# Kernel tuning notes

Measured on AMD Instinct MI355X. Metric: run time of the kernel, lower is better.

The kernel has to match this reference:

```python
import jax, jax.numpy as jnp
import numpy as np

B, T, HW = 16, 64, 7
D = 768          # input_dim == base_dim
N = 12           # num_heads
C = D // N       # head_dim = 64
EPS = 1e-5


def layernorm(x, g, b):
    m = jnp.mean(x, axis=-1, keepdims=True)
    v = jnp.mean((x - m) ** 2, axis=-1, keepdims=True)
    return (x - m) * jax.lax.rsqrt(v + EPS) * g + b


def setup_inputs() -> dict:
    key = jax.random.key(0)
    ks = jax.random.split(key, 12)
    s = lambda k, shape: (jax.random.normal(k, shape, jnp.float32) * 0.02)
    return {
        "x": jax.random.normal(ks[0], (B, T, HW, HW, D), jnp.float32),
        "W_qkv": s(ks[1], (D, 3 * D)),                  # qkv_bias=False
        "Wpq": s(ks[2], (C, C, HW, HW)), "bpq": jnp.zeros((C,), jnp.float32),
        "Wpk": s(ks[3], (C, C, HW, HW)), "bpk": jnp.zeros((C,), jnp.float32),
        "Wpv": s(ks[4], (C, C, HW, HW)), "bpv": jnp.zeros((C,), jnp.float32),
        "g_q": jnp.ones((C,), jnp.float32), "be_q": jnp.zeros((C,), jnp.float32),
        "g_k": jnp.ones((C,), jnp.float32), "be_k": jnp.zeros((C,), jnp.float32),
        "g_v": jnp.ones((C,), jnp.float32), "be_v": jnp.zeros((C,), jnp.float32),
        "rel_pos_t": s(ks[5], (2 * T - 1, C)),          # (127, 64): matches dt, no interp
        "W_proj": s(ks[6], (D, D)), "b_proj": jnp.zeros((D,), jnp.float32),
    }


def reference(x, W_qkv, Wpq, bpq, Wpk, bpk, Wpv, bpv,
              g_q, be_q, g_k, be_k, g_v, be_v, rel_pos_t, W_proj, b_proj):
    b, t = x.shape[0], x.shape[1]
    # qkv projection -> (B,T,H,W,3,N,C)
    qkv = (x @ W_qkv).reshape(b, t, HW, HW, 3, N, C)
    q3, k3, v3 = qkv[..., 0, :, :], qkv[..., 1, :, :], qkv[..., 2, :, :]  # (B,T,H,W,N,C)
    # Conv3d kernel (1,7,7) on full 7x7 spatial == contraction over (h,w,c_in)
    q = jnp.einsum('bthwnc,dchw->bntd', q3, Wpq) + bpq   # (B,N,T,C)
    k = jnp.einsum('bthwnc,dchw->bntd', k3, Wpk) + bpk
    v = jnp.einsum('bthwnc,dchw->bntd', v3, Wpv) + bpv
    q = layernorm(q, g_q, be_q)
    k = layernorm(k, g_k, be_k)
    v = layernorm(v, g_v, be_v)
    scale = C ** -0.5
    attn = jnp.einsum('bntc,bnsc->bnts', q * scale, k)   # (B,N,T,T)
    # relative temporal position bias: gather table rows by distance, matmul with q
    dist = jnp.arange(t)[:, None] - jnp.arange(t)[None, :] + (t - 1)  # (T,T) in [0,2T-2]
    Rt = rel_pos_t[dist]                                  # (T,T,C)
    rel = jnp.einsum('bntc,tsc->bnts', q, Rt)
    attn = jax.nn.softmax(attn + rel, axis=-1)
    out = jnp.einsum('bnts,bnsc->bntc', attn, v) + q      # residual add of q
    out = out.transpose(0, 2, 1, 3).reshape(b, t, N * C)  # (B,T,D)
    return out @ W_proj + b_proj
```

## Files before the change

kernel.cpp:

```cpp
#include <hip/hip_runtime.h>


typedef __attribute__((ext_vector_type(8))) short bf16x8;
typedef __attribute__((ext_vector_type(4))) float f32x4;

#define AS1U(p) ((const __attribute__((address_space(1))) unsigned int*)(p))
#define AS3U(p) ((__attribute__((address_space(3))) unsigned int*)(p))

__device__ __forceinline__ unsigned short cvt_bf16(float x) {
  union { float f; unsigned int u; } v; v.f = x;
  unsigned int r = v.u + 0x7fffu + ((v.u >> 16) & 1u);
  return (unsigned short)(r >> 16);
}
__device__ __forceinline__ float bf2f(unsigned short h) {
  union { unsigned int u; float f; } v; v.u = ((unsigned int)h) << 16;
  return v.f;
}

__device__ __forceinline__ void wg_barrier() {
  asm volatile("" ::: "memory");
  __builtin_amdgcn_s_barrier();
  asm volatile("" ::: "memory");
}

__global__ __launch_bounds__(256) void cvt_x_k(const float* __restrict__ src,
                                               unsigned short* __restrict__ dst, int n8) {
  int i = blockIdx.x * 256 + threadIdx.x;
  if (i >= n8) return;
  const float4* s = (const float4*)src + (size_t)i * 2;
  float4 a = s[0], b = s[1];
  ushort4 r0 = { cvt_bf16(a.x), cvt_bf16(a.y), cvt_bf16(a.z), cvt_bf16(a.w) };
  ushort4 r1 = { cvt_bf16(b.x), cvt_bf16(b.y), cvt_bf16(b.z), cvt_bf16(b.w) };
  ushort4* d = (ushort4*)dst + (size_t)i * 2;
  d[0] = r0; d[1] = r1;
}

__global__ __launch_bounds__(256) void transpose_cvt_k(const float* __restrict__ src,
                                                       unsigned short* __restrict__ dst) {
  __shared__ float tl[32][33];
  int k0 = blockIdx.x * 32, n0 = blockIdx.y * 32;
  int tx = threadIdx.x & 31, ty = threadIdx.x >> 5;
#pragma unroll
  for (int r = 0; r < 32; r += 8)
    tl[ty + r][tx] = src[(size_t)(k0 + ty + r) * 2304 + n0 + tx];
  __syncthreads();
#pragma unroll
  for (int r = 0; r < 32; r += 8)
    dst[(size_t)(n0 + ty + r) * 768 + k0 + tx] = cvt_bf16(tl[tx][ty + r]);
}

__global__ __launch_bounds__(256) void wp_cvt_k(const float* __restrict__ src,
                                                unsigned short* __restrict__ dst) {
  int o = blockIdx.x * 256 + threadIdx.x;
  if (o >= 204800) return;
  int c = o & 63, d = (o >> 6) & 63, hw = o >> 12;
  dst[o] = (hw < 49) ? cvt_bf16(src[d * 3136 + c * 49 + hw]) : (unsigned short)0;
}

__global__ __launch_bounds__(256) void relp_cvt_k(const float* __restrict__ src,
                                                  unsigned short* __restrict__ dst) {
  int i = blockIdx.x * 256 + threadIdx.x;
  if (i >= 8192) return;
  dst[i] = (i < 8128) ? cvt_bf16(src[i]) : (unsigned short)0;
}

__global__ __launch_bounds__(512, 2) void gemm_qkv_8ph(
    const unsigned short* __restrict__ A, const unsigned short* __restrict__ Bt,
    unsigned short* __restrict__ Cb) {
  __shared__ unsigned short As[2][16384];
  __shared__ unsigned short Bs[2][16384];

  const int orig = blockIdx.x;
  const int xcd = orig & 7;
  const int lid = orig >> 3;
  const int wgid = (xcd < 4 ? xcd * 221 : 884 + (xcd - 4) * 220) + lid;
  const int mb = wgid / 9, nb = wgid % 9;
  const int m0 = mb * 256, n0 = nb * 256;
  const int K = 768;

  const int tid = threadIdx.x;
  const int wave = tid >> 6, lane = tid & 63;
  const int quad = lane >> 4, l16 = lane & 15;
  const int wr = wave >> 2, wc = wave & 3;
  const int x7 = l16 & 7;

  const int srow = tid >> 3;
  const int cs = (tid & 7) ^ (srow & 7);
  const unsigned short* Ag[4];
  const unsigned short* Bg[4];
#pragma unroll
  for (int l = 0; l < 4; ++l) {
    Ag[l] = A + (size_t)(m0 + l * 64 + srow) * K + cs * 8;
    Bg[l] = Bt + (size_t)(n0 + l * 64 + srow) * K + cs * 8;
  }
  const int ldst = wave * 512;

#define STAGE(buf, kt) do {                                                        \
    const int ko_ = (kt) * 64;                                                     \
    _Pragma("unroll")                                                              \
    for (int l_ = 0; l_ < 4; ++l_) {                                               \
      __builtin_amdgcn_global_load_lds(AS1U(Ag[l_] + ko_),                         \
          AS3U(&As[buf][l_ * 4096 + ldst]), 16, 0, 0);                             \
      __builtin_amdgcn_global_load_lds(AS1U(Bg[l_] + ko_),                         \
          AS3U(&Bs[buf][l_ * 4096 + ldst]), 16, 0, 0);                             \
    }                                                                              \
  } while (0)

#define LDA(buf, mi) do {                                                          \
    _Pragma("unroll")                                                              \
    for (int fi_ = 0; fi_ < 4; ++fi_) {                                            \
      const int row_ = wr * 128 + (mi) * 64 + fi_ * 16 + l16;                      \
      _Pragma("unroll")                                                            \
      for (int ks_ = 0; ks_ < 2; ++ks_)                                            \
        af[fi_][ks_] = *(const bf16x8*)&As[buf][row_ * 64 +                        \
            (((ks_ * 4 + quad) ^ x7) * 8)];                                        \
    }                                                                              \
  } while (0)

#define LDB(buf, nj) do {                                                          \
    _Pragma("unroll")                                                              \
    for (int fj_ = 0; fj_ < 2; ++fj_) {                                            \
      const int row_ = wc * 64 + (nj) * 32 + fj_ * 16 + l16;                       \
      _Pragma("unroll")                                                            \
      for (int ks_ = 0; ks_ < 2; ++ks_)                                            \
        bfv[nj][fj_][ks_] = *(const bf16x8*)&Bs[buf][row_ * 64 +                   \
            (((ks_ * 4 + quad) ^ x7) * 8)];                                        \
    }                                                                              \
  } while (0)

#define MFMAQ(mi, nj) do {                                                         \
    _Pragma("unroll")                                                              \
    for (int ks_ = 0; ks_ < 2; ++ks_)                                              \
      _Pragma("unroll")                                                            \
      for (int fi_ = 0; fi_ < 4; ++fi_)                                            \
        _Pragma("unroll")                                                          \
        for (int fj_ = 0; fj_ < 2; ++fj_)                                          \
          acc[(mi) * 4 + fi_][(nj) * 2 + fj_] =                                    \
              __builtin_amdgcn_mfma_f32_16x16x32_bf16(af[fi_][ks_],                \
                  bfv[nj][fj_][ks_], acc[(mi) * 4 + fi_][(nj) * 2 + fj_], 0, 0, 0);\
  } while (0)

#define ITER(cur, DO_STAGE, kt2, VMI) do {                                         \
    asm volatile("s_waitcnt vmcnt(" #VMI ")" ::: "memory");                        \
    wg_barrier();                                                                  \
                                                                           \
    LDA(cur, 0); LDB(cur, 0);                                                      \
    wg_barrier();                                                                  \
    __builtin_amdgcn_s_setprio(1); MFMAQ(0, 0); __builtin_amdgcn_s_setprio(0);     \
    wg_barrier();                                                                  \
                                                                           \
    LDB(cur, 1);                                                                   \
    wg_barrier();                                                                  \
    __builtin_amdgcn_s_setprio(1); MFMAQ(0, 1); __builtin_amdgcn_s_setprio(0);     \
    wg_barrier();                                                                  \
                                                                           \
    LDA(cur, 1);                                                                   \
    wg_barrier();                                                                  \
    __builtin_amdgcn_s_setprio(1); MFMAQ(1, 0); __builtin_amdgcn_s_setprio(0);     \
    wg_barrier();                                                                  \
             \
    if (DO_STAGE) STAGE(cur, kt2);                                                 \
    __builtin_amdgcn_s_setprio(1); MFMAQ(1, 1); __builtin_amdgcn_s_setprio(0);     \
    wg_barrier();                                                                  \
  } while (0)

  f32x4 acc[8][4];
#pragma unroll
  for (int i = 0; i < 8; ++i)
#pragma unroll
    for (int j = 0; j < 4; ++j) acc[i][j] = (f32x4){0.f, 0.f, 0.f, 0.f};
  bf16x8 af[4][2];
  bf16x8 bfv[2][2][2];

  STAGE(0, 0);
  STAGE(1, 1);

  for (int kt = 0; kt < 10; kt += 2) {
    ITER(0, true, kt + 2, 8);
    ITER(1, true, kt + 3, 8);
  }
  ITER(0, false, 0, 8);
  ITER(1, false, 0, 0);

#undef ITER
#undef MFMAQ
#undef LDB
#undef LDA
#undef STAGE

#pragma unroll
  for (int i = 0; i < 8; ++i)
#pragma unroll
    for (int j = 0; j < 4; ++j)
#pragma unroll
      for (int r = 0; r < 4; ++r) {
        int row = m0 + wr * 128 + i * 16 + quad * 4 + r;
        int col = n0 + wc * 64 + j * 16 + l16;
        Cb[(size_t)row * 2304 + col] = cvt_bf16(acc[i][j][r]);
      }
}

__global__ __launch_bounds__(256) void pool_ln_mfma_k(
    const unsigned short* __restrict__ qkvb, const unsigned short* __restrict__ WpTT,
    const float* __restrict__ bq, const float* __restrict__ bk, const float* __restrict__ bv,
    const float* __restrict__ gq, const float* __restrict__ gk, const float* __restrict__ gv,
    const float* __restrict__ beq, const float* __restrict__ bek, const float* __restrict__ bev,
    unsigned short* __restrict__ oq, unsigned short* __restrict__ ok_,
    unsigned short* __restrict__ ov) {
  __shared__ unsigned short As[64 * 128];
  __shared__ unsigned short Bs[64 * 128];
  __shared__ float Ln[64 * 65];
  __shared__ float mu_s[64], rs_s[64];

  const int n = blockIdx.x, p = blockIdx.y, b = blockIdx.z;
  const int tid = threadIdx.x;
  const int wave = tid >> 6, lane = tid & 63;
  const int quad = lane >> 4, l16 = lane & 15;
  const int wm = (wave >> 1) * 32, wn = (wave & 1) * 32;

  const int lr = lane >> 4, lg = lane & 15;
  const size_t abase = ((size_t)b * 3136) * 2304 + (size_t)p * 768 + (size_t)n * 64;
  const unsigned short* WpB = WpTT + (size_t)p * 204800;

  const unsigned short* pA[4];
  const unsigned short* pB[4];
#pragma unroll
  for (int q = 0; q < 4; ++q) {
    int r = wave * 16 + q * 4 + lr;
    int g = lg ^ (r & 15);
    pA[q] = qkvb + abase + (size_t)r * 112896 + (size_t)(g >> 3) * 2304 + (g & 7) * 8;
    pB[q] = WpB + (size_t)(g >> 3) * 4096 + r * 64 + (g & 7) * 8;
  }

  f32x4 acc[2][2];
#pragma unroll
  for (int i = 0; i < 2; ++i)
#pragma unroll
    for (int j = 0; j < 2; ++j) acc[i][j] = (f32x4){0.f, 0.f, 0.f, 0.f};

  for (int it = 0; it < 25; ++it) {
    const size_t offA = (size_t)it * 4608;
    const size_t offB = (size_t)it * 8192;
#pragma unroll
    for (int q = 0; q < 4; ++q) {
      __builtin_amdgcn_global_load_lds(AS1U(pA[q] + offA), AS3U(&As[(wave * 16 + q * 4) * 128]), 16, 0, 0);
      __builtin_amdgcn_global_load_lds(AS1U(pB[q] + offB), AS3U(&Bs[(wave * 16 + q * 4) * 128]), 16, 0, 0);
    }
    __syncthreads();
    bf16x8 af[2][4], bfr[2][4];
#pragma unroll
    for (int f = 0; f < 2; ++f) {
      int ra = wm + f * 16 + l16;
      int rb = wn + f * 16 + l16;
#pragma unroll
      for (int ki = 0; ki < 4; ++ki) {
        af[f][ki]  = *(const bf16x8*)&As[ra * 128 + (((ki * 4 + quad) ^ (ra & 15)) * 8)];
        bfr[f][ki] = *(const bf16x8*)&Bs[rb * 128 + (((ki * 4 + quad) ^ (rb & 15)) * 8)];
      }
    }
#pragma unroll
    for (int ki = 0; ki < 4; ++ki)
#pragma unroll
      for (int i = 0; i < 2; ++i)
#pragma unroll
        for (int j = 0; j < 2; ++j)
          acc[i][j] = __builtin_amdgcn_mfma_f32_16x16x32_bf16(af[i][ki], bfr[j][ki], acc[i][j], 0, 0, 0);
    __syncthreads();
  }

  const float* bias = (p == 0) ? bq : (p == 1) ? bk : bv;
  const float* g    = (p == 0) ? gq : (p == 1) ? gk : gv;
  const float* be   = (p == 0) ? beq : (p == 1) ? bek : bev;
  unsigned short* outp = (p == 0) ? oq : (p == 1) ? ok_ : ov;

#pragma unroll
  for (int i = 0; i < 2; ++i)
#pragma unroll
    for (int j = 0; j < 2; ++j)
#pragma unroll
      for (int r = 0; r < 4; ++r) {
        int t = wm + i * 16 + quad * 4 + r;
        int d = wn + j * 16 + l16;
        Ln[t * 65 + d] = acc[i][j][r] + bias[d];
      }
  __syncthreads();
  if (tid < 64) {
    float s = 0.f;
#pragma unroll 8
    for (int c = 0; c < 64; ++c) s += Ln[tid * 65 + c];
    float m = s * (1.f / 64.f);
    float v2 = 0.f;
#pragma unroll 8
    for (int c = 0; c < 64; ++c) { float dl = Ln[tid * 65 + c] - m; v2 += dl * dl; }
    mu_s[tid] = m;
    rs_s[tid] = rsqrtf(v2 * (1.f / 64.f) + 1e-5f);
  }
  __syncthreads();
  {
    int t = tid >> 2, d0 = (tid & 3) * 16;
    float m = mu_s[t], rv = rs_s[t];
    unsigned short ob[16];
#pragma unroll
    for (int j = 0; j < 16; ++j)
      ob[j] = cvt_bf16((Ln[t * 65 + d0 + j] - m) * rv * g[d0 + j] + be[d0 + j]);
    unsigned short* dst = outp + ((size_t)(b * 12 + n) * 64 + t) * 64 + d0;
    *(uint4*)dst = *(uint4*)ob;
    *(uint4*)(dst + 8) = *(uint4*)(ob + 8);
  }
}

__global__ __launch_bounds__(256) void attn_mfma_k(
    const unsigned short* __restrict__ qp, const unsigned short* __restrict__ kp,
    const unsigned short* __restrict__ vp, const unsigned short* __restrict__ relb,
    float* __restrict__ aout) {
  __shared__ unsigned short qs[64 * 64];
  __shared__ unsigned short ks[64 * 64];
  __shared__ unsigned short vt[64 * 64];
  __shared__ unsigned short rs[128 * 64];
  __shared__ float Gs[64 * 128];
  __shared__ unsigned short Ps[64 * 64];

  const int n = blockIdx.x, b = blockIdx.y;
  const int tid = threadIdx.x;
  const size_t base = ((size_t)b * 12 + n) * 4096;

  for (int i = tid; i < 512; i += 256) {
    ((uint4*)qs)[i] = ((const uint4*)(qp + base))[i];
    ((uint4*)ks)[i] = ((const uint4*)(kp + base))[i];
  }
  for (int i = tid; i < 1024; i += 256)
    ((uint4*)rs)[i] = ((const uint4*)relb)[i];
  {
    int s = tid >> 2, c0 = (tid & 3) * 16;
    unsigned short tmp[16];
    *(uint4*)tmp = *(const uint4*)(vp + base + s * 64 + c0);
    *(uint4*)(tmp + 8) = *(const uint4*)(vp + base + s * 64 + c0 + 8);
#pragma unroll
    for (int i = 0; i < 16; ++i) vt[(c0 + i) * 64 + s] = tmp[i];
  }
  __syncthreads();

  const int wave = tid >> 6, lane = tid & 63;
  const int quad = lane >> 4, l16 = lane & 15;
  const int tm = wave * 16;

  bf16x8 aq[2];
  aq[0] = *(const bf16x8*)&qs[(tm + l16) * 64 + quad * 8];
  aq[1] = *(const bf16x8*)&qs[(tm + l16) * 64 + quad * 8 + 32];

  f32x4 accqk[4], accg[8];
#pragma unroll
  for (int j = 0; j < 4; ++j) accqk[j] = (f32x4){0.f, 0.f, 0.f, 0.f};
#pragma unroll
  for (int j = 0; j < 8; ++j) accg[j] = (f32x4){0.f, 0.f, 0.f, 0.f};

#pragma unroll
  for (int ki = 0; ki < 2; ++ki) {
#pragma unroll
    for (int j = 0; j < 4; ++j) {
      bf16x8 bk = *(const bf16x8*)&ks[(j * 16 + l16) * 64 + quad * 8 + ki * 32];
      accqk[j] = __builtin_amdgcn_mfma_f32_16x16x32_bf16(aq[ki], bk, accqk[j], 0, 0, 0);
    }
#pragma unroll
    for (int j = 0; j < 8; ++j) {
      bf16x8 br = *(const bf16x8*)&rs[(j * 16 + l16) * 64 + quad * 8 + ki * 32];
      accg[j] = __builtin_amdgcn_mfma_f32_16x16x32_bf16(aq[ki], br, accg[j], 0, 0, 0);
    }
  }
#pragma unroll
  for (int j = 0; j < 8; ++j)
#pragma unroll
    for (int r = 0; r < 4; ++r)
      Gs[(tm + quad * 4 + r) * 128 + j * 16 + l16] = accg[j][r];
  __syncthreads();

#pragma unroll
  for (int r = 0; r < 4; ++r) {
    int t = tm + quad * 4 + r;
    float sv[4];
#pragma unroll
    for (int j = 0; j < 4; ++j) {
      int s = j * 16 + l16;
      sv[j] = 0.125f * accqk[j][r] + Gs[t * 128 + (t + 63 - s)];
    }
    float m = fmaxf(fmaxf(sv[0], sv[1]), fmaxf(sv[2], sv[3]));
    m = fmaxf(m, __shfl_xor(m, 1));
    m = fmaxf(m, __shfl_xor(m, 2));
    m = fmaxf(m, __shfl_xor(m, 4));
    m = fmaxf(m, __shfl_xor(m, 8));
    float e[4], sum = 0.f;
#pragma unroll
    for (int j = 0; j < 4; ++j) { e[j] = __expf(sv[j] - m); sum += e[j]; }
    sum += __shfl_xor(sum, 1);
    sum += __shfl_xor(sum, 2);
    sum += __shfl_xor(sum, 4);
    sum += __shfl_xor(sum, 8);
    float inv = 1.f / sum;
#pragma unroll
    for (int j = 0; j < 4; ++j)
      Ps[t * 64 + j * 16 + l16] = cvt_bf16(e[j] * inv);
  }
  __syncthreads();

  bf16x8 ap[2];
  ap[0] = *(const bf16x8*)&Ps[(tm + l16) * 64 + quad * 8];
  ap[1] = *(const bf16x8*)&Ps[(tm + l16) * 64 + quad * 8 + 32];
  f32x4 acco[4];
#pragma unroll
  for (int j = 0; j < 4; ++j) acco[j] = (f32x4){0.f, 0.f, 0.f, 0.f};
#pragma unroll
  for (int ki = 0; ki < 2; ++ki)
#pragma unroll
    for (int j = 0; j < 4; ++j) {
      bf16x8 bv = *(const bf16x8*)&vt[(j * 16 + l16) * 64 + quad * 8 + ki * 32];
      acco[j] = __builtin_amdgcn_mfma_f32_16x16x32_bf16(ap[ki], bv, acco[j], 0, 0, 0);
    }
#pragma unroll
  for (int j = 0; j < 4; ++j)
#pragma unroll
    for (int r = 0; r < 4; ++r) {
      int t = tm + quad * 4 + r;
      int c = j * 16 + l16;
      float o = acco[j][r] + bf2f(qs[t * 64 + c]);
      aout[((size_t)b * 64 + t) * 768 + n * 64 + c] = o;
    }
}

__global__ __launch_bounds__(256) void gemm_f32_k(
    const float* __restrict__ A, const float* __restrict__ Bm,
    const float* __restrict__ bias, float* __restrict__ Cm,
    int M, int Nn, int K) {
  __shared__ float As[16][68];
  __shared__ float Bs[16][64];
  const int tid = threadIdx.x;
  const int ty = tid >> 4, tx = tid & 15;
  const int m0 = blockIdx.y * 64, n0 = blockIdx.x * 64;

  const int la_m = tid >> 2;
  const int la_k = (tid & 3) << 2;
  const int lb_k = tid >> 4;
  const int lb_n = (tid & 15) << 2;

  const float* Ap = A + (size_t)(m0 + la_m) * K + la_k;
  const float* Bp = Bm + (size_t)lb_k * Nn + n0 + lb_n;

  float acc[4][4];
#pragma unroll
  for (int i = 0; i < 4; ++i)
#pragma unroll
    for (int j = 0; j < 4; ++j) acc[i][j] = 0.f;

  for (int k0 = 0; k0 < K; k0 += 16) {
    float4 av = *(const float4*)(Ap + k0);
    float4 bv = *(const float4*)(Bp + (size_t)k0 * Nn);
    As[la_k + 0][la_m] = av.x;
    As[la_k + 1][la_m] = av.y;
    As[la_k + 2][la_m] = av.z;
    As[la_k + 3][la_m] = av.w;
    *(float4*)&Bs[lb_k][lb_n] = bv;
    __syncthreads();
#pragma unroll
    for (int kk = 0; kk < 16; ++kk) {
      float af[4], bf[4];
      *(float4*)af = *(const float4*)&As[kk][ty << 2];
      *(float4*)bf = *(const float4*)&Bs[kk][tx << 2];
#pragma unroll
      for (int i = 0; i < 4; ++i)
#pragma unroll
        for (int j = 0; j < 4; ++j) acc[i][j] += af[i] * bf[j];
    }
    __syncthreads();
  }

  float bb[4] = {0.f, 0.f, 0.f, 0.f};
  if (bias) {
#pragma unroll
    for (int j = 0; j < 4; ++j) bb[j] = bias[n0 + (tx << 2) + j];
  }
#pragma unroll
  for (int i = 0; i < 4; ++i) {
    float4 o;
    o.x = acc[i][0] + bb[0];
    o.y = acc[i][1] + bb[1];
    o.z = acc[i][2] + bb[2];
    o.w = acc[i][3] + bb[3];
    *(float4*)(Cm + (size_t)(m0 + (ty << 2) + i) * Nn + n0 + (tx << 2)) = o;
  }
}

extern "C" void kernel_launch(void* const* d_in, const int* in_sizes, int n_in,
                              void* d_out, int out_size, void* d_ws, size_t ws_size,
                              hipStream_t stream) {
  const float* x     = (const float*)d_in[0];
  const float* Wqkv  = (const float*)d_in[1];
  const float* Wpq   = (const float*)d_in[2];
  const float* bpq   = (const float*)d_in[3];
  const float* Wpk   = (const float*)d_in[4];
  const float* bpk   = (const float*)d_in[5];
  const float* Wpv   = (const float*)d_in[6];
  const float* bpv   = (const float*)d_in[7];
  const float* gq    = (const float*)d_in[8];
  const float* beq   = (const float*)d_in[9];
  const float* gk    = (const float*)d_in[10];
  const float* bek   = (const float*)d_in[11];
  const float* gv    = (const float*)d_in[12];
  const float* bev   = (const float*)d_in[13];
  const float* relp  = (const float*)d_in[14];
  const float* Wproj = (const float*)d_in[15];
  const float* bproj = (const float*)d_in[16];
  float* out = (float*)d_out;

  unsigned short* u = (unsigned short*)d_ws;
  unsigned short* xbf   = u;
  unsigned short* qkvbf = u + 38535168ull;
  unsigned short* WqkvT = u + 154140672ull;
  unsigned short* WpTT  = u + 155910144ull;
  unsigned short* relb  = u + 156524544ull;
  unsigned short* qpb   = u + 156532736ull;
  unsigned short* kpb   = u + 157319168ull;
  unsigned short* vpb   = u + 158105600ull;
  float* aout = (float*)(u + 158892032ull);

  cvt_x_k<<<18816, 256, 0, stream>>>(x, xbf, 4816896);
  transpose_cvt_k<<<dim3(24, 72), 256, 0, stream>>>(Wqkv, WqkvT);
  wp_cvt_k<<<800, 256, 0, stream>>>(Wpq, WpTT);
  wp_cvt_k<<<800, 256, 0, stream>>>(Wpk, WpTT + 204800);
  wp_cvt_k<<<800, 256, 0, stream>>>(Wpv, WpTT + 409600);
  relp_cvt_k<<<32, 256, 0, stream>>>(relp, relb);

  gemm_qkv_8ph<<<1764, 512, 0, stream>>>(xbf, WqkvT, qkvbf);

  pool_ln_mfma_k<<<dim3(12, 3, 16), 256, 0, stream>>>(
      qkvbf, WpTT, bpq, bpk, bpv, gq, gk, gv, beq, bek, bev, qpb, kpb, vpb);

  attn_mfma_k<<<dim3(12, 16), 256, 0, stream>>>(qpb, kpb, vpb, relb, aout);

  gemm_f32_k<<<dim3(12, 16), 256, 0, stream>>>(aout, Wproj, bproj, out, 1024, 768, 768);
}
```

Baseline: 614.6 us.

## Stage QKV GEMM epilogue through LDS, merge prep kernels, prefetch proj GEMM

Measured after the change: 632.8 us. 3.0% more time.

```diff
diff --git a/kernel.cpp b/kernel.cpp
--- a/kernel.cpp
+++ b/kernel.cpp
@@ -49,26 +49,29 @@
     dst[(size_t)(n0 + ty + r) * 768 + k0 + tx] = cvt_bf16(tl[tx][ty + r]);
 }
 
-__global__ __launch_bounds__(256) void wp_cvt_k(const float* __restrict__ src,
-                                                unsigned short* __restrict__ dst) {
-  int o = blockIdx.x * 256 + threadIdx.x;
-  if (o >= 204800) return;
-  int c = o & 63, d = (o >> 6) & 63, hw = o >> 12;
-  dst[o] = (hw < 49) ? cvt_bf16(src[d * 3136 + c * 49 + hw]) : (unsigned short)0;
-}
-
-__global__ __launch_bounds__(256) void relp_cvt_k(const float* __restrict__ src,
-                                                  unsigned short* __restrict__ dst) {
-  int i = blockIdx.x * 256 + threadIdx.x;
-  if (i >= 8192) return;
-  dst[i] = (i < 8128) ? cvt_bf16(src[i]) : (unsigned short)0;
+__global__ __launch_bounds__(256) void prep_cvt_k(
+    const float* __restrict__ Wpq, const float* __restrict__ Wpk,
+    const float* __restrict__ Wpv, const float* __restrict__ relp,
+    unsigned short* __restrict__ WpTT, unsigned short* __restrict__ relb) {
+  int bid = blockIdx.x;
+  if (bid < 2400) {
+    int p = bid / 800;
+    const float* src = (p == 0) ? Wpq : (p == 1) ? Wpk : Wpv;
+    unsigned short* dst = WpTT + (size_t)p * 204800;
+    int o = (bid - p * 800) * 256 + threadIdx.x;
+    if (o >= 204800) return;
+    int c = o & 63, d = (o >> 6) & 63, hw = o >> 12;
+    dst[o] = (hw < 49) ? cvt_bf16(src[d * 3136 + c * 49 + hw]) : (unsigned short)0;
+  } else {
+    int i = (bid - 2400) * 256 + threadIdx.x;
+    relb[i] = (i < 8128) ? cvt_bf16(relp[i]) : (unsigned short)0;
+  }
 }
 
 __global__ __launch_bounds__(512, 2) void gemm_qkv_8ph(
     const unsigned short* __restrict__ A, const unsigned short* __restrict__ Bt,
     unsigned short* __restrict__ Cb) {
-  __shared__ unsigned short As[2][16384];
-  __shared__ unsigned short Bs[2][16384];
+  __shared__ unsigned short smem[65536];
 
   const int orig = blockIdx.x;
   const int xcd = orig & 7;
@@ -100,9 +103,9 @@
     _Pragma("unroll")                                                              \
     for (int l_ = 0; l_ < 4; ++l_) {                                               \
       __builtin_amdgcn_global_load_lds(AS1U(Ag[l_] + ko_),                         \
-          AS3U(&As[buf][l_ * 4096 + ldst]), 16, 0, 0);                             \
+          AS3U(&smem[(buf) * 16384 + l_ * 4096 + ldst]), 16, 0, 0);                \
       __builtin_amdgcn_global_load_lds(AS1U(Bg[l_] + ko_),                         \
-          AS3U(&Bs[buf][l_ * 4096 + ldst]), 16, 0, 0);                             \
+          AS3U(&smem[32768 + (buf) * 16384 + l_ * 4096 + ldst]), 16, 0, 0);        \
     }                                                                              \
   } while (0)
 
@@ -112,7 +115,7 @@
       const int row_ = wr * 128 + (mi) * 64 + fi_ * 16 + l16;                      \
       _Pragma("unroll")                                                            \
       for (int ks_ = 0; ks_ < 2; ++ks_)                                            \
-        af[fi_][ks_] = *(const bf16x8*)&As[buf][row_ * 64 +                        \
+        af[fi_][ks_] = *(const bf16x8*)&smem[(buf) * 16384 + row_ * 64 +           \
             (((ks_ * 4 + quad) ^ x7) * 8)];                                        \
     }                                                                              \
   } while (0)
@@ -123,8 +126,8 @@
       const int row_ = wc * 64 + (nj) * 32 + fj_ * 16 + l16;                       \
       _Pragma("unroll")                                                            \
       for (int ks_ = 0; ks_ < 2; ++ks_)                                            \
-        bfv[nj][fj_][ks_] = *(const bf16x8*)&Bs[buf][row_ * 64 +                   \
-            (((ks_ * 4 + quad) ^ x7) * 8)];                                        \
+        bfv[nj][fj_][ks_] = *(const bf16x8*)&smem[32768 + (buf) * 16384 +          \
+            row_ * 64 + (((ks_ * 4 + quad) ^ x7) * 8)];                            \
     }                                                                              \
   } while (0)
 
@@ -194,10 +197,23 @@
     for (int j = 0; j < 4; ++j)
 #pragma unroll
       for (int r = 0; r < 4; ++r) {
-        int row = m0 + wr * 128 + i * 16 + quad * 4 + r;
-        int col = n0 + wc * 64 + j * 16 + l16;
-        Cb[(size_t)row * 2304 + col] = cvt_bf16(acc[i][j][r]);
+        int row = wr * 128 + i * 16 + quad * 4 + r;
+        int col = wc * 64 + j * 16 + l16;
+        smem[row * 256 + ((((col >> 3) ^ (row & 7)) << 3) | (col & 7))] =
+            cvt_bf16(acc[i][j][r]);
       }
+  wg_barrier();
+  {
+    const int r2 = tid >> 1;
+    const int cb2 = (tid & 1) * 16;
+    unsigned short* crow = Cb + (size_t)(m0 + r2) * 2304 + n0;
+#pragma unroll
+    for (int q = 0; q < 16; ++q) {
+      int c = cb2 + q;
+      bf16x8 v = *(const bf16x8*)&smem[r2 * 256 + ((c ^ (r2 & 7)) << 3)];
+      *(bf16x8*)(crow + c * 8) = v;
+    }
+  }
 }
 
 __global__ __launch_bounds__(256) void pool_ln_mfma_k(
@@ -450,15 +466,19 @@
 #pragma unroll
     for (int j = 0; j < 4; ++j) acc[i][j] = 0.f;
 
+  float4 av = *(const float4*)(Ap);
+  float4 bv = *(const float4*)(Bp);
   for (int k0 = 0; k0 < K; k0 += 16) {
-    float4 av = *(const float4*)(Ap + k0);
-    float4 bv = *(const float4*)(Bp + (size_t)k0 * Nn);
     As[la_k + 0][la_m] = av.x;
     As[la_k + 1][la_m] = av.y;
     As[la_k + 2][la_m] = av.z;
     As[la_k + 3][la_m] = av.w;
     *(float4*)&Bs[lb_k][lb_n] = bv;
     __syncthreads();
+    if (k0 + 16 < K) {
+      av = *(const float4*)(Ap + k0 + 16);
+      bv = *(const float4*)(Bp + (size_t)(k0 + 16) * Nn);
+    }
 #pragma unroll
     for (int kk = 0; kk < 16; ++kk) {
       float af[4], bf[4];
@@ -523,10 +543,7 @@
 
   cvt_x_k<<<18816, 256, 0, stream>>>(x, xbf, 4816896);
   transpose_cvt_k<<<dim3(24, 72), 256, 0, stream>>>(Wqkv, WqkvT);
-  wp_cvt_k<<<800, 256, 0, stream>>>(Wpq, WpTT);
-  wp_cvt_k<<<800, 256, 0, stream>>>(Wpk, WpTT + 204800);
-  wp_cvt_k<<<800, 256, 0, stream>>>(Wpv, WpTT + 409600);
-  relp_cvt_k<<<32, 256, 0, stream>>>(relp, relb);
+  prep_cvt_k<<<2432, 256, 0, stream>>>(Wpq, Wpk, Wpv, relp, WpTT, relb);
 
   gemm_qkv_8ph<<<1764, 512, 0, stream>>>(xbf, WqkvT, qkvbf);
 
```
